# Optimization experiments

Hardware: AMD Instinct MI355X
Metric: run time of the kernel (lower is better)

The kernel has to match this reference:

```python
import jax, jax.numpy as jnp
import numpy as np

NIN, NHID, NDECHID, NOUT = 128, 256, 512, 10
B, N = 32, 4096


def _linear_params(key, fan_in, fan_out):
    kw, kb = jax.random.split(key)
    bound = 1.0 / np.sqrt(fan_in)
    W = jax.random.uniform(kw, (fan_in, fan_out), jnp.float32, -bound, bound)
    b = jax.random.uniform(kb, (fan_out,), jnp.float32, -bound, bound)
    return W, b


def setup_inputs() -> dict:
    key = jax.random.key(0)
    ks = jax.random.split(key, 7)
    x = jax.random.normal(ks[0], (B, N, NIN), jnp.float32)
    W1, b1 = _linear_params(ks[1], NIN, NHID)
    W2, b2 = _linear_params(ks[2], NHID, NHID)
    W3, b3 = _linear_params(ks[3], NHID, NHID)
    D1, c1 = _linear_params(ks[4], NHID, NDECHID)
    D2, c2 = _linear_params(ks[5], NDECHID, NDECHID)
    D3, c3 = _linear_params(ks[6], NDECHID, NOUT)
    return {"x": x, "W1": W1, "b1": b1, "W2": W2, "b2": b2, "W3": W3, "b3": b3,
            "D1": D1, "c1": c1, "D2": D2, "c2": c2, "D3": D3, "c3": c3}


def reference(x, W1, b1, W2, b2, W3, b3, D1, c1, D2, c2, D3, c3):
    # encoder MLP: Linear-ReLU-Linear-ReLU-Linear, then extra ReLU
    h = jax.nn.relu(x @ W1 + b1)            # [B, N, nhid]
    h = jax.nn.relu(h @ W2 + b2)
    h = jax.nn.relu(h @ W3 + b3)            # fused enc output + F.relu
    # mean_{i,j}(h_i * h_j) over the set == (mean_i h)^2 elementwise (exact identity)
    m = jnp.mean(h, axis=1)                  # [B, nhid]
    p = jax.nn.relu(m * m)                   # [B, nhid]
    # decoder MLP
    d = jax.nn.relu(p @ D1 + c1)
    d = jax.nn.relu(d @ D2 + c2)
    return d @ D3 + c3                       # [B, nout]
```

## Files before the change

### kernel.cpp

```cpp
#include <hip/hip_runtime.h>
#include <hip/hip_bf16.h>
#include <stdint.h>


#define NIN   128
#define NHID  256
#define NDEC  512
#define NOUTC 10
#define BATCH 32
#define NTOK  4096
#define MTILE 64
#define NBLK  (BATCH * (NTOK / MTILE))
#define XPAD  136
#define HPAD  264

typedef short bf16x8 __attribute__((ext_vector_type(8)));
typedef float floatx4 __attribute__((ext_vector_type(4)));

__device__ __forceinline__ uint16_t f2b(float f) {
  union { uint32_t u; float f; } v; v.f = f;
  uint32_t r = v.u + 0x7FFFu + ((v.u >> 16) & 1u);
  return (uint16_t)(r >> 16);
}
__device__ __forceinline__ uint32_t pkbf(float lo, float hi) {
  __hip_bfloat162 h = __float22bfloat162_rn(float2{lo, hi});
  union { __hip_bfloat162 h; uint32_t u; } c; c.h = h;
  return c.u;
}

__global__ __launch_bounds__(256) void pack_weights(
    const float* __restrict__ W1, const float* __restrict__ W2,
    const float* __restrict__ W3, uint16_t* __restrict__ pW,
    float* __restrict__ msum) {
  int p = blockIdx.x * blockDim.x + threadIdx.x;
  if (p < BATCH * NHID) msum[p] = 0.f;
  const float* W; int K; int base;
  if (p < 32768)      { W = W1; K = NIN;  base = 0; }
  else if (p < 98304) { W = W2; K = NHID; base = 32768; p -= 32768; }
  else                { W = W3; K = NHID; base = 98304; p -= 98304; }
  int j    = p & 7;
  int ln   = (p >> 3) & 63;
  int rest = p >> 9;
  int KC = K >> 5;
  int kc = rest % KC;
  int mt = rest / KC;
  int m = mt * 16 + (ln & 15);
  int k = kc * 32 + ((ln >> 4) << 3) + j;
  pW[base + (((mt * KC + kc) * 64 + ln) << 3) + j] = f2b(W[k * NHID + m]);
}

__global__ __launch_bounds__(256) void encoder(
    const float* __restrict__ x,
    const uint16_t* __restrict__ pW,
    const float* __restrict__ b1,
    const float* __restrict__ b2,
    const float* __restrict__ b3,
    float* __restrict__ msum) {
  __shared__ __align__(16) uint16_t Hs[MTILE * HPAD];

  const int tid  = threadIdx.x;
  const int wave = tid >> 6;
  const int lane = tid & 63;
  const int l15  = lane & 15;
  const int q    = lane >> 4;
  const int tok0  = blockIdx.x * MTILE;
  const int batch = blockIdx.x >> 6;

  const uint16_t* pW1 = pW;
  const uint16_t* pW2 = pW + 32768;
  const uint16_t* pW3 = pW + 98304;

  {
    const int row = tid >> 2;
    const int c0  = (tid & 3) * 32;
    const float* xr = x + (size_t)(tok0 + row) * NIN + c0;
    for (int i = 0; i < 8; ++i) {
      float4 v = *(const float4*)(xr + i * 4);
      uint2 u = make_uint2(pkbf(v.x, v.y), pkbf(v.z, v.w));
      *(uint2*)&Hs[row * XPAD + c0 + i * 4] = u;
    }
  }
  __syncthreads();

  floatx4 acc[4][4];

  for (int jt = 0; jt < 4; ++jt)
    for (int tt = 0; tt < 4; ++tt)
      acc[jt][tt] = (floatx4){0.f, 0.f, 0.f, 0.f};
#pragma unroll
  for (int kc = 0; kc < 4; ++kc) {
    bf16x8 a[4], b[4];
#pragma unroll
    for (int jt = 0; jt < 4; ++jt)
      a[jt] = *(const bf16x8*)(pW1 + ((((wave * 4 + jt) * 4 + kc) * 64 + lane) << 3));
#pragma unroll
    for (int tt = 0; tt < 4; ++tt)
      b[tt] = *(const bf16x8*)&Hs[(tt * 16 + l15) * XPAD + kc * 32 + q * 8];
#pragma unroll
    for (int jt = 0; jt < 4; ++jt)
#pragma unroll
      for (int tt = 0; tt < 4; ++tt)
        acc[jt][tt] = __builtin_amdgcn_mfma_f32_16x16x32_bf16(
            a[jt], b[tt], acc[jt][tt], 0, 0, 0);
  }
  __syncthreads();

#pragma unroll
  for (int jt = 0; jt < 4; ++jt) {
    const int jbase = wave * 64 + jt * 16 + q * 4;
    const float4 bb = *(const float4*)&b1[jbase];
#pragma unroll
    for (int tt = 0; tt < 4; ++tt) {
      const int t = tt * 16 + l15;
      float v0 = fmaxf(acc[jt][tt][0] + bb.x, 0.f);
      float v1 = fmaxf(acc[jt][tt][1] + bb.y, 0.f);
      float v2 = fmaxf(acc[jt][tt][2] + bb.z, 0.f);
      float v3 = fmaxf(acc[jt][tt][3] + bb.w, 0.f);
      *(uint2*)&Hs[t * HPAD + jbase] = make_uint2(pkbf(v0, v1), pkbf(v2, v3));
    }
  }
  __syncthreads();

  for (int jt = 0; jt < 4; ++jt)
    for (int tt = 0; tt < 4; ++tt)
      acc[jt][tt] = (floatx4){0.f, 0.f, 0.f, 0.f};
#pragma unroll
  for (int kc = 0; kc < 8; ++kc) {
    bf16x8 a[4], b[4];
#pragma unroll
    for (int jt = 0; jt < 4; ++jt)
      a[jt] = *(const bf16x8*)(pW2 + ((((wave * 4 + jt) * 8 + kc) * 64 + lane) << 3));
#pragma unroll
    for (int tt = 0; tt < 4; ++tt)
      b[tt] = *(const bf16x8*)&Hs[(tt * 16 + l15) * HPAD + kc * 32 + q * 8];
#pragma unroll
    for (int jt = 0; jt < 4; ++jt)
#pragma unroll
      for (int tt = 0; tt < 4; ++tt)
        acc[jt][tt] = __builtin_amdgcn_mfma_f32_16x16x32_bf16(
            a[jt], b[tt], acc[jt][tt], 0, 0, 0);
  }
  __syncthreads();
#pragma unroll
  for (int jt = 0; jt < 4; ++jt) {
    const int jbase = wave * 64 + jt * 16 + q * 4;
    const float4 bb = *(const float4*)&b2[jbase];
#pragma unroll
    for (int tt = 0; tt < 4; ++tt) {
      const int t = tt * 16 + l15;
      float v0 = fmaxf(acc[jt][tt][0] + bb.x, 0.f);
      float v1 = fmaxf(acc[jt][tt][1] + bb.y, 0.f);
      float v2 = fmaxf(acc[jt][tt][2] + bb.z, 0.f);
      float v3 = fmaxf(acc[jt][tt][3] + bb.w, 0.f);
      *(uint2*)&Hs[t * HPAD + jbase] = make_uint2(pkbf(v0, v1), pkbf(v2, v3));
    }
  }
  __syncthreads();

  for (int jt = 0; jt < 4; ++jt)
    for (int tt = 0; tt < 4; ++tt)
      acc[jt][tt] = (floatx4){0.f, 0.f, 0.f, 0.f};
#pragma unroll
  for (int kc = 0; kc < 8; ++kc) {
    bf16x8 a[4], b[4];
#pragma unroll
    for (int jt = 0; jt < 4; ++jt)
      a[jt] = *(const bf16x8*)(pW3 + ((((wave * 4 + jt) * 8 + kc) * 64 + lane) << 3));
#pragma unroll
    for (int tt = 0; tt < 4; ++tt)
      b[tt] = *(const bf16x8*)&Hs[(tt * 16 + l15) * HPAD + kc * 32 + q * 8];
#pragma unroll
    for (int jt = 0; jt < 4; ++jt)
#pragma unroll
      for (int tt = 0; tt < 4; ++tt)
        acc[jt][tt] = __builtin_amdgcn_mfma_f32_16x16x32_bf16(
            a[jt], b[tt], acc[jt][tt], 0, 0, 0);
  }
  __syncthreads();

  {
    float4* scratch = (float4*)Hs;
#pragma unroll
    for (int jt = 0; jt < 4; ++jt) {
      const int jbase = wave * 64 + jt * 16 + q * 4;
      const float4 bb = *(const float4*)&b3[jbase];
      float s0 = 0.f, s1 = 0.f, s2 = 0.f, s3 = 0.f;
#pragma unroll
      for (int tt = 0; tt < 4; ++tt) {
        s0 += fmaxf(acc[jt][tt][0] + bb.x, 0.f);
        s1 += fmaxf(acc[jt][tt][1] + bb.y, 0.f);
        s2 += fmaxf(acc[jt][tt][2] + bb.z, 0.f);
        s3 += fmaxf(acc[jt][tt][3] + bb.w, 0.f);
      }
      scratch[((wave * 4 + jt) * 4 + q) * 17 + l15] = (float4){s0, s1, s2, s3};
    }
  }
  __syncthreads();
  {
    const int c = tid >> 2;
    const int r = tid & 3;
    const float* sf = (const float*)Hs;
    float v = 0.f;
#pragma unroll
    for (int l = 0; l < 16; ++l)
      v += sf[c * 68 + l * 4 + r];
    const int wv = c >> 4, jt = (c >> 2) & 3, qq = c & 3;
    const int j = wv * 64 + jt * 16 + qq * 4 + r;
    atomicAdd(&msum[batch * NHID + j], v);
  }
}

__global__ __launch_bounds__(1024) void decoder(
    const float* __restrict__ msum,
    const float* __restrict__ D1, const float* __restrict__ c1,
    const float* __restrict__ D2, const float* __restrict__ c2,
    const float* __restrict__ D3, const float* __restrict__ c3,
    float* __restrict__ out) {
  __shared__ float p[NHID];
  __shared__ float d1[NDEC];
  __shared__ float d2[NDEC];
  __shared__ __align__(16) float red[4096];
  const int b = blockIdx.x, t = threadIdx.x;

  if (t < NHID) {
    float m = msum[b * NHID + t] * (1.f / NTOK);
    p[t] = m * m;
  }
  __syncthreads();

  const int jg = t & 127;
  const int ks = t >> 7;

  {
    const float4* D1v = (const float4*)D1;
    float4 s = {0.f, 0.f, 0.f, 0.f};
    for (int k = ks * 32; k < ks * 32 + 32; ++k) {
      float4 w = D1v[k * 128 + jg];
      float pv = p[k];
      s.x += pv * w.x; s.y += pv * w.y; s.z += pv * w.z; s.w += pv * w.w;
    }
    *(float4*)&red[t * 4] = s;
    __syncthreads();
    if (t < NDEC) {
      float v = c1[t];
#pragma unroll
      for (int i = 0; i < 8; ++i) v += red[i * 512 + t];
      d1[t] = fmaxf(v, 0.f);
    }
    __syncthreads();
  }

  {
    const float4* D2v = (const float4*)D2;
    float4 s = {0.f, 0.f, 0.f, 0.f};
    for (int k = ks * 64; k < ks * 64 + 64; ++k) {
      float4 w = D2v[k * 128 + jg];
      float hv = d1[k];
      s.x += hv * w.x; s.y += hv * w.y; s.z += hv * w.z; s.w += hv * w.w;
    }
    *(float4*)&red[t * 4] = s;
    __syncthreads();
    if (t < NDEC) {
      float v = c2[t];
#pragma unroll
      for (int i = 0; i < 8; ++i) v += red[i * 512 + t];
      d2[t] = fmaxf(v, 0.f);
    }
    __syncthreads();
  }

  {
    const int j3 = t & 15;
    const int kc = t >> 4;
    float s = 0.f;
    if (j3 < NOUTC)
      for (int k = kc * 8; k < kc * 8 + 8; ++k)
        s += d2[k] * D3[k * NOUTC + j3];
    red[t] = s;
    __syncthreads();
    if (t < NOUTC) {
      float v = c3[t];
#pragma unroll
      for (int i = 0; i < 64; ++i) v += red[i * 16 + t];
      out[b * NOUTC + t] = v;
    }
  }
}

extern "C" void kernel_launch(void* const* d_in, const int* in_sizes, int n_in,
                              void* d_out, int out_size, void* d_ws, size_t ws_size,
                              hipStream_t stream) {
  const float* x  = (const float*)d_in[0];
  const float* W1 = (const float*)d_in[1];
  const float* b1 = (const float*)d_in[2];
  const float* W2 = (const float*)d_in[3];
  const float* b2 = (const float*)d_in[4];
  const float* W3 = (const float*)d_in[5];
  const float* b3 = (const float*)d_in[6];
  const float* D1 = (const float*)d_in[7];
  const float* c1 = (const float*)d_in[8];
  const float* D2 = (const float*)d_in[9];
  const float* c2 = (const float*)d_in[10];
  const float* D3 = (const float*)d_in[11];
  const float* c3 = (const float*)d_in[12];

  uint16_t* pW   = (uint16_t*)d_ws;
  float*    msum = (float*)((char*)d_ws + 384 * 1024);

  pack_weights<<<640, 256, 0, stream>>>(W1, W2, W3, pW, msum);
  encoder<<<NBLK, 256, 0, stream>>>(x, pW, b1, b2, b3, msum);
  decoder<<<BATCH, 1024, 0, stream>>>(msum, D1, c1, D2, c2, D3, c3,
                                      (float*)d_out);
}
```

Measured before the change: 173.8 us.

## Swizzle encoder LDS layout, fold bias into accumulator init, split decoder across blocks

Replaces the padded LDS activation layout with an XOR-swizzled byte layout and coalesces the x tile load into 32-byte chunks per thread. Bias is now loaded into the MFMA accumulator init, which removes the bias add from each epilogue. The decoder is split into 4 blocks per batch that each handle a quarter of the D2 outputs and combine their D3 contributions with atomics; out is pre-initialized with c3 in the pack kernel. This trades more decoder parallelism for atomic accumulation and float summation-order nondeterminism.

```diff
diff --git a/kernel.cpp b/kernel.cpp
--- a/kernel.cpp
+++ b/kernel.cpp
@@ -11,8 +11,8 @@
 #define NTOK  4096
 #define MTILE 64
 #define NBLK  (BATCH * (NTOK / MTILE))
-#define XPAD  136
-#define HPAD  264
+
+#define SWZ(t) (((t) & 7) << 4)
 
 typedef short bf16x8 __attribute__((ext_vector_type(8)));
 typedef float floatx4 __attribute__((ext_vector_type(4)));
@@ -30,10 +30,12 @@
 
 __global__ __launch_bounds__(256) void pack_weights(
     const float* __restrict__ W1, const float* __restrict__ W2,
-    const float* __restrict__ W3, uint16_t* __restrict__ pW,
-    float* __restrict__ msum) {
+    const float* __restrict__ W3, const float* __restrict__ c3,
+    uint16_t* __restrict__ pW, float* __restrict__ msum,
+    float* __restrict__ out) {
   int p = blockIdx.x * blockDim.x + threadIdx.x;
   if (p < BATCH * NHID) msum[p] = 0.f;
+  if (p < BATCH * NOUTC) out[p] = c3[p % NOUTC];
   const float* W; int K; int base;
   if (p < 32768)      { W = W1; K = NIN;  base = 0; }
   else if (p < 98304) { W = W2; K = NHID; base = 32768; p -= 32768; }
@@ -56,7 +58,7 @@
     const float* __restrict__ b2,
     const float* __restrict__ b3,
     float* __restrict__ msum) {
-  __shared__ __align__(16) uint16_t Hs[MTILE * HPAD];
+  __shared__ __align__(16) uint8_t Hs[MTILE * 512];
 
   const int tid  = threadIdx.x;
   const int wave = tid >> 6;
@@ -71,22 +73,30 @@
   const uint16_t* pW3 = pW + 98304;
 
   {
-    const int row = tid >> 2;
-    const int c0  = (tid & 3) * 32;
-    const float* xr = x + (size_t)(tok0 + row) * NIN + c0;
-    for (int i = 0; i < 8; ++i) {
-      float4 v = *(const float4*)(xr + i * 4);
-      uint2 u = make_uint2(pkbf(v.x, v.y), pkbf(v.z, v.w));
-      *(uint2*)&Hs[row * XPAD + c0 + i * 4] = u;
+    const float4* xv = (const float4*)(x + (size_t)tok0 * NIN);
+#pragma unroll
+    for (int i = 0; i < 4; ++i) {
+      const int u = tid + i * 256;
+      float4 va = xv[2 * u];
+      float4 vb = xv[2 * u + 1];
+      uint4 w = make_uint4(pkbf(va.x, va.y), pkbf(va.z, va.w),
+                           pkbf(vb.x, vb.y), pkbf(vb.z, vb.w));
+      const int row = u >> 4;
+      const int cb  = (u & 15) << 4;
+      *(uint4*)&Hs[row * 256 + (cb ^ SWZ(row))] = w;
     }
   }
   __syncthreads();
 
   floatx4 acc[4][4];
 
-  for (int jt = 0; jt < 4; ++jt)
+#pragma unroll
+  for (int jt = 0; jt < 4; ++jt) {
+    const float4 bb = *(const float4*)&b1[wave * 64 + jt * 16 + q * 4];
+#pragma unroll
     for (int tt = 0; tt < 4; ++tt)
-      acc[jt][tt] = (floatx4){0.f, 0.f, 0.f, 0.f};
+      acc[jt][tt] = (floatx4){bb.x, bb.y, bb.z, bb.w};
+  }
 #pragma unroll
   for (int kc = 0; kc < 4; ++kc) {
     bf16x8 a[4], b[4];
@@ -94,8 +104,10 @@
     for (int jt = 0; jt < 4; ++jt)
       a[jt] = *(const bf16x8*)(pW1 + ((((wave * 4 + jt) * 4 + kc) * 64 + lane) << 3));
 #pragma unroll
-    for (int tt = 0; tt < 4; ++tt)
-      b[tt] = *(const bf16x8*)&Hs[(tt * 16 + l15) * XPAD + kc * 32 + q * 8];
+    for (int tt = 0; tt < 4; ++tt) {
+      const int t = tt * 16 + l15;
+      b[tt] = *(const bf16x8*)&Hs[t * 256 + ((kc * 64 + q * 16) ^ SWZ(t))];
+    }
 #pragma unroll
     for (int jt = 0; jt < 4; ++jt)
 #pragma unroll
@@ -107,23 +119,26 @@
 
 #pragma unroll
   for (int jt = 0; jt < 4; ++jt) {
-    const int jbase = wave * 64 + jt * 16 + q * 4;
-    const float4 bb = *(const float4*)&b1[jbase];
-#pragma unroll
-    for (int tt = 0; tt < 4; ++tt) {
-      const int t = tt * 16 + l15;
-      float v0 = fmaxf(acc[jt][tt][0] + bb.x, 0.f);
-      float v1 = fmaxf(acc[jt][tt][1] + bb.y, 0.f);
-      float v2 = fmaxf(acc[jt][tt][2] + bb.z, 0.f);
-      float v3 = fmaxf(acc[jt][tt][3] + bb.w, 0.f);
-      *(uint2*)&Hs[t * HPAD + jbase] = make_uint2(pkbf(v0, v1), pkbf(v2, v3));
-    }
-  }
-  __syncthreads();
-
-  for (int jt = 0; jt < 4; ++jt)
+    const int cb = (wave * 64 + jt * 16 + q * 4) * 2;
+#pragma unroll
+    for (int tt = 0; tt < 4; ++tt) {
+      const int t = tt * 16 + l15;
+      float v0 = fmaxf(acc[jt][tt][0], 0.f);
+      float v1 = fmaxf(acc[jt][tt][1], 0.f);
+      float v2 = fmaxf(acc[jt][tt][2], 0.f);
+      float v3 = fmaxf(acc[jt][tt][3], 0.f);
+      *(uint2*)&Hs[t * 512 + (cb ^ SWZ(t))] = make_uint2(pkbf(v0, v1), pkbf(v2, v3));
+    }
+  }
+  __syncthreads();
+
+#pragma unroll
+  for (int jt = 0; jt < 4; ++jt) {
+    const float4 bb = *(const float4*)&b2[wave * 64 + jt * 16 + q * 4];
+#pragma unroll
     for (int tt = 0; tt < 4; ++tt)
-      acc[jt][tt] = (floatx4){0.f, 0.f, 0.f, 0.f};
+      acc[jt][tt] = (floatx4){bb.x, bb.y, bb.z, bb.w};
+  }
 #pragma unroll
   for (int kc = 0; kc < 8; ++kc) {
     bf16x8 a[4], b[4];
@@ -131,8 +146,10 @@
     for (int jt = 0; jt < 4; ++jt)
       a[jt] = *(const bf16x8*)(pW2 + ((((wave * 4 + jt) * 8 + kc) * 64 + lane) << 3));
 #pragma unroll
-    for (int tt = 0; tt < 4; ++tt)
-      b[tt] = *(const bf16x8*)&Hs[(tt * 16 + l15) * HPAD + kc * 32 + q * 8];
+    for (int tt = 0; tt < 4; ++tt) {
+      const int t = tt * 16 + l15;
+      b[tt] = *(const bf16x8*)&Hs[t * 512 + ((kc * 64 + q * 16) ^ SWZ(t))];
+    }
 #pragma unroll
     for (int jt = 0; jt < 4; ++jt)
 #pragma unroll
@@ -143,23 +160,26 @@
   __syncthreads();
 #pragma unroll
   for (int jt = 0; jt < 4; ++jt) {
-    const int jbase = wave * 64 + jt * 16 + q * 4;
-    const float4 bb = *(const float4*)&b2[jbase];
-#pragma unroll
-    for (int tt = 0; tt < 4; ++tt) {
-      const int t = tt * 16 + l15;
-      float v0 = fmaxf(acc[jt][tt][0] + bb.x, 0.f);
-      float v1 = fmaxf(acc[jt][tt][1] + bb.y, 0.f);
-      float v2 = fmaxf(acc[jt][tt][2] + bb.z, 0.f);
-      float v3 = fmaxf(acc[jt][tt][3] + bb.w, 0.f);
-      *(uint2*)&Hs[t * HPAD + jbase] = make_uint2(pkbf(v0, v1), pkbf(v2, v3));
-    }
-  }
-  __syncthreads();
-
-  for (int jt = 0; jt < 4; ++jt)
+    const int cb = (wave * 64 + jt * 16 + q * 4) * 2;
+#pragma unroll
+    for (int tt = 0; tt < 4; ++tt) {
+      const int t = tt * 16 + l15;
+      float v0 = fmaxf(acc[jt][tt][0], 0.f);
+      float v1 = fmaxf(acc[jt][tt][1], 0.f);
+      float v2 = fmaxf(acc[jt][tt][2], 0.f);
+      float v3 = fmaxf(acc[jt][tt][3], 0.f);
+      *(uint2*)&Hs[t * 512 + (cb ^ SWZ(t))] = make_uint2(pkbf(v0, v1), pkbf(v2, v3));
+    }
+  }
+  __syncthreads();
+
+#pragma unroll
+  for (int jt = 0; jt < 4; ++jt) {
+    const float4 bb = *(const float4*)&b3[wave * 64 + jt * 16 + q * 4];
+#pragma unroll
     for (int tt = 0; tt < 4; ++tt)
-      acc[jt][tt] = (floatx4){0.f, 0.f, 0.f, 0.f};
+      acc[jt][tt] = (floatx4){bb.x, bb.y, bb.z, bb.w};
+  }
 #pragma unroll
   for (int kc = 0; kc < 8; ++kc) {
     bf16x8 a[4], b[4];
@@ -167,8 +187,10 @@
     for (int jt = 0; jt < 4; ++jt)
       a[jt] = *(const bf16x8*)(pW3 + ((((wave * 4 + jt) * 8 + kc) * 64 + lane) << 3));
 #pragma unroll
-    for (int tt = 0; tt < 4; ++tt)
-      b[tt] = *(const bf16x8*)&Hs[(tt * 16 + l15) * HPAD + kc * 32 + q * 8];
+    for (int tt = 0; tt < 4; ++tt) {
+      const int t = tt * 16 + l15;
+      b[tt] = *(const bf16x8*)&Hs[t * 512 + ((kc * 64 + q * 16) ^ SWZ(t))];
+    }
 #pragma unroll
     for (int jt = 0; jt < 4; ++jt)
 #pragma unroll
@@ -182,15 +204,13 @@
     float4* scratch = (float4*)Hs;
 #pragma unroll
     for (int jt = 0; jt < 4; ++jt) {
-      const int jbase = wave * 64 + jt * 16 + q * 4;
-      const float4 bb = *(const float4*)&b3[jbase];
       float s0 = 0.f, s1 = 0.f, s2 = 0.f, s3 = 0.f;
 #pragma unroll
       for (int tt = 0; tt < 4; ++tt) {
-        s0 += fmaxf(acc[jt][tt][0] + bb.x, 0.f);
-        s1 += fmaxf(acc[jt][tt][1] + bb.y, 0.f);
-        s2 += fmaxf(acc[jt][tt][2] + bb.z, 0.f);
-        s3 += fmaxf(acc[jt][tt][3] + bb.w, 0.f);
+        s0 += fmaxf(acc[jt][tt][0], 0.f);
+        s1 += fmaxf(acc[jt][tt][1], 0.f);
+        s2 += fmaxf(acc[jt][tt][2], 0.f);
+        s3 += fmaxf(acc[jt][tt][3], 0.f);
       }
       scratch[((wave * 4 + jt) * 4 + q) * 17 + l15] = (float4){s0, s1, s2, s3};
     }
@@ -214,13 +234,13 @@
     const float* __restrict__ msum,
     const float* __restrict__ D1, const float* __restrict__ c1,
     const float* __restrict__ D2, const float* __restrict__ c2,
-    const float* __restrict__ D3, const float* __restrict__ c3,
+    const float* __restrict__ D3,
     float* __restrict__ out) {
   __shared__ float p[NHID];
   __shared__ float d1[NDEC];
-  __shared__ float d2[NDEC];
+  __shared__ float d2q[128];
   __shared__ __align__(16) float red[4096];
-  const int b = blockIdx.x, t = threadIdx.x;
+  const int b = blockIdx.x >> 2, qd = blockIdx.x & 3, t = threadIdx.x;
 
   if (t < NHID) {
     float m = msum[b * NHID + t] * (1.f / NTOK);
@@ -228,10 +248,9 @@
   }
   __syncthreads();
 
-  const int jg = t & 127;
-  const int ks = t >> 7;
-
-  {
+  {
+    const int jg = t & 127;
+    const int ks = t >> 7;
     const float4* D1v = (const float4*)D1;
     float4 s = {0.f, 0.f, 0.f, 0.f};
     for (int k = ks * 32; k < ks * 32 + 32; ++k) {
@@ -251,20 +270,22 @@
   }
 
   {
+    const int jg2 = t & 31;
+    const int ks2 = t >> 5;
     const float4* D2v = (const float4*)D2;
     float4 s = {0.f, 0.f, 0.f, 0.f};
-    for (int k = ks * 64; k < ks * 64 + 64; ++k) {
-      float4 w = D2v[k * 128 + jg];
+    for (int k = ks2 * 16; k < ks2 * 16 + 16; ++k) {
+      float4 w = D2v[k * 128 + qd * 32 + jg2];
       float hv = d1[k];
       s.x += hv * w.x; s.y += hv * w.y; s.z += hv * w.z; s.w += hv * w.w;
     }
     *(float4*)&red[t * 4] = s;
     __syncthreads();
-    if (t < NDEC) {
-      float v = c2[t];
-#pragma unroll
-      for (int i = 0; i < 8; ++i) v += red[i * 512 + t];
-      d2[t] = fmaxf(v, 0.f);
+    if (t < 128) {
+      float v = c2[qd * 128 + t];
+#pragma unroll
+      for (int i = 0; i < 32; ++i) v += red[i * 128 + t];
+      d2q[t] = fmaxf(v, 0.f);
     }
     __syncthreads();
   }
@@ -274,15 +295,15 @@
     const int kc = t >> 4;
     float s = 0.f;
     if (j3 < NOUTC)
-      for (int k = kc * 8; k < kc * 8 + 8; ++k)
-        s += d2[k] * D3[k * NOUTC + j3];
+      for (int k = kc * 2; k < kc * 2 + 2; ++k)
+        s += d2q[k] * D3[(qd * 128 + k) * NOUTC + j3];
     red[t] = s;
     __syncthreads();
     if (t < NOUTC) {
-      float v = c3[t];
+      float v = 0.f;
 #pragma unroll
       for (int i = 0; i < 64; ++i) v += red[i * 16 + t];
-      out[b * NOUTC + t] = v;
+      atomicAdd(&out[b * NOUTC + t], v);
     }
   }
 }
@@ -307,8 +328,9 @@
   uint16_t* pW   = (uint16_t*)d_ws;
   float*    msum = (float*)((char*)d_ws + 384 * 1024);
 
-  pack_weights<<<640, 256, 0, stream>>>(W1, W2, W3, pW, msum);
+  pack_weights<<<640, 256, 0, stream>>>(W1, W2, W3, c3, pW, msum,
+                                        (float*)d_out);
   encoder<<<NBLK, 256, 0, stream>>>(x, pW, b1, b2, b3, msum);
-  decoder<<<BATCH, 1024, 0, stream>>>(msum, D1, c1, D2, c2, D3, c3,
-                                      (float*)d_out);
-}
+  decoder<<<128, 1024, 0, stream>>>(msum, D1, c1, D2, c2, D3,
+                                    (float*)d_out);
+}
```

Result: faster. 159.6 us (-8.2%).
